# Optimization experiments

Measured on AMD Instinct MI355X. Metric: run time of the kernel, lower is better.

## Reference

```python
import jax, jax.numpy as jnp
import numpy as np


def setup_inputs() -> dict:
    key = jax.random.key(0)
    ks = jax.random.split(key, 6)
    B, N, Cd, Qd, E, G = 256, 196, 2048, 1024, 1024, 8
    s = lambda d: 1.0 / np.sqrt(d)
    return {
        "context": jax.random.normal(ks[0], (B, N, Cd), dtype=jnp.float32),
        "query": jax.random.normal(ks[1], (B, Qd), dtype=jnp.float32),
        "Wq": jax.random.normal(ks[2], (E, Qd), dtype=jnp.float32) * s(Qd),
        "bq": jnp.zeros((E,), dtype=jnp.float32),
        "Wc": jax.random.normal(ks[3], (E, Cd), dtype=jnp.float32) * s(Cd),
        "bc": jnp.zeros((E,), dtype=jnp.float32),
        "Wo": jax.random.normal(ks[4], (G, E), dtype=jnp.float32) * s(E),
        "bo": jnp.zeros((G,), dtype=jnp.float32),
    }


def reference(context, query, Wq, bq, Wc, bc, Wo, bo):
    # query: [B, Qd] -> [B, 1, E]; context: [B, N, Cd] -> [B, N, E]
    qp = (query @ Wq.T + bq)[:, None, :]
    cp = jnp.einsum('bnc,ec->bne', context, Wc) + bc
    # dropout in eval mode (identity)
    combined = jnp.tanh(qp + cp)                      # [B, N, E]
    attn = jnp.einsum('bne,ge->bng', combined, Wo) + bo  # [B, N, G]
    weights = jax.nn.softmax(attn, axis=1)            # softmax over regions
    glimpses = jnp.einsum('bng,bnc->bgc', weights, context)  # [B, G, Cd]
    return glimpses.reshape(context.shape[0], -1)     # [B, G*Cd]
```

## Files before the change

### kernel.cpp

```cpp
#include <hip/hip_runtime.h>
#include <stdint.h>

typedef unsigned int u32;
typedef __bf16 bf16_t;
typedef bf16_t bf16x8 __attribute__((ext_vector_type(8)));
typedef bf16_t bf16x4 __attribute__((ext_vector_type(4)));
typedef float  f32x4  __attribute__((ext_vector_type(4)));

#define NB   256
#define NN   196
#define CD   2048
#define QD   1024
#define NE   1024
#define NG   8

#define WS_QP    0
#define WS_ATTN  (NB*NE*4)
#define WS_WCB   (WS_ATTN + NB*NG*NN*4)

__device__ __forceinline__ bf16_t f2bf(float f){
  u32 u = __float_as_uint(f);
  u += 0x7fffu + ((u >> 16) & 1u);
  unsigned short h = (unsigned short)(u >> 16);
  return __builtin_bit_cast(bf16_t, h);
}

__device__ __forceinline__ float fast_tanh(float x){
  float e = __expf(2.0f * x);
  return 1.0f - 2.0f / (e + 1.0f);
}

__device__ __forceinline__ void load_lds16(const void* g, void* l){
  __builtin_amdgcn_global_load_lds(
      (const __attribute__((address_space(1))) void*)g,
      (__attribute__((address_space(3))) void*)l, 16, 0, 0);
}

__global__ __launch_bounds__(256)
void k_conv(const float* __restrict__ src, bf16_t* __restrict__ dst){
  size_t i = ((size_t)blockIdx.x * 256 + threadIdx.x) * 4;
  float4 v = *(const float4*)(src + i);
  bf16x4 o = { f2bf(v.x), f2bf(v.y), f2bf(v.z), f2bf(v.w) };
  *(bf16x4*)(dst + i) = o;
}

__global__ __launch_bounds__(256)
void k_qp(const float* __restrict__ query, const float* __restrict__ Wq,
          const float* __restrict__ bq, float* __restrict__ qp){
  __shared__ float qs[32][36];
  __shared__ float wsm[32][36];
  const u32 t  = threadIdx.x;
  const u32 e0 = blockIdx.x * 32, b0 = blockIdx.y * 32;
  const u32 r  = t >> 3, ci = (t & 7) * 4;
  const u32 tm = (t >> 4) * 2, tn = (t & 15) * 2;
  float c00 = 0.f, c01 = 0.f, c10 = 0.f, c11 = 0.f;
  for (u32 k0 = 0; k0 < QD; k0 += 32){
    float4 qv = *(const float4*)(query + (size_t)(b0 + r) * QD + k0 + ci);
    float4 wv = *(const float4*)(Wq    + (size_t)(e0 + r) * QD + k0 + ci);
    __syncthreads();
    *(float4*)&qs[r][ci]  = qv;
    *(float4*)&wsm[r][ci] = wv;
    __syncthreads();
    #pragma unroll
    for (int kq = 0; kq < 8; kq++){
      float4 a0 = *(const float4*)&qs[tm][kq*4];
      float4 a1 = *(const float4*)&qs[tm+1][kq*4];
      float4 b0v = *(const float4*)&wsm[tn][kq*4];
      float4 b1v = *(const float4*)&wsm[tn+1][kq*4];
      c00 += a0.x*b0v.x + a0.y*b0v.y + a0.z*b0v.z + a0.w*b0v.w;
      c01 += a0.x*b1v.x + a0.y*b1v.y + a0.z*b1v.z + a0.w*b1v.w;
      c10 += a1.x*b0v.x + a1.y*b0v.y + a1.z*b0v.z + a1.w*b0v.w;
      c11 += a1.x*b1v.x + a1.y*b1v.y + a1.z*b1v.z + a1.w*b1v.w;
    }
  }
  float bq0 = bq[e0+tn], bq1 = bq[e0+tn+1];
  qp[(size_t)(b0+tm  )*NE + e0+tn  ] = c00 + bq0;
  qp[(size_t)(b0+tm  )*NE + e0+tn+1] = c01 + bq1;
  qp[(size_t)(b0+tm+1)*NE + e0+tn  ] = c10 + bq0;
  qp[(size_t)(b0+tm+1)*NE + e0+tn+1] = c11 + bq1;
}

#define BM 128
#define BN 128
#define BK 32
#define KSTEPS (CD/BK)

__global__ __launch_bounds__(256, 3)
void k_mainA(const float* __restrict__ ctx, const bf16_t* __restrict__ wcb,
             const float* __restrict__ qp, const float* __restrict__ bcv,
             const float* __restrict__ Wo, float* __restrict__ attn)
{
  __shared__ char smem[49152] __attribute__((aligned(128)));

  const u32 tid  = threadIdx.x;
  const u32 lane = tid & 63;
  const u32 wave = tid >> 6;
  const u32 wm   = wave >> 1;
  const u32 wn   = wave & 1;

  u32 d  = blockIdx.x;
  u32 x  = d & 7;
  u32 s  = d >> 3;
  u32 ec = s & 7;
  u32 j  = s >> 3;
  u32 ms = j * 8 + x;
  const u32 m0 = ms * BM;
  const u32 e0 = ec * BN;

  const u32 arow = tid >> 3;
  const u32 aq   = (tid & 7) ^ (arow & 7);
  const float* aS = ctx + (size_t)(m0 + arow) * CD + aq * 4;
  char* aD = smem + tid * 16;

  const u32 brow0 = tid >> 2;
  const u32 brow1 = (tid + 256) >> 2;
  const u32 bkq0  = (tid & 3) ^ ((tid >> 3) & 3);
  const u32 bkq1  = (tid & 3) ^ (((tid + 256) >> 3) & 3);
  const bf16_t* bS0 = wcb + (size_t)(e0 + brow0) * CD + bkq0 * 8;
  const bf16_t* bS1 = wcb + (size_t)(e0 + brow1) * CD + bkq1 * 8;
  char* bD0 = smem + 32768 + tid * 16;
  char* bD1 = bD0 + 4096;

  f32x4 acc[4][4];
  #pragma unroll
  for (int i = 0; i < 4; i++)
    #pragma unroll
    for (int jn = 0; jn < 4; jn++) acc[i][jn] = (f32x4){0.f,0.f,0.f,0.f};

  auto stage = [&](u32 buf, u32 ks){
    const u32 ko = ks * BK;
    #pragma unroll
    for (int p = 0; p < 4; p++)
      load_lds16(aS + (size_t)(p * 32) * CD + ko, aD + buf * 16384u + p * 4096u);
    load_lds16(bS0 + ko, bD0 + buf * 8192u);
    load_lds16(bS1 + ko, bD1 + buf * 8192u);
  };

  const u32 q   = lane >> 4;
  const u32 r15 = lane & 15;
  const u32 as0 = ((2*q)     ^ (r15 & 7)) * 16;
  const u32 as1 = ((2*q + 1) ^ (r15 & 7)) * 16;
  const u32 bsw = (q ^ ((r15 >> 1) & 3)) * 16;

  auto compute = [&](u32 buf){
    const char* A = smem + buf * 16384u;
    const char* B = smem + 32768u + buf * 8192u;
    bf16x8 af[4], bfr[4];
    #pragma unroll
    for (int mt = 0; mt < 4; mt++){
      u32 row = wm*64 + mt*16 + r15;
      const char* rb = A + row * 128u;
      f32x4 lo = *(const f32x4*)(rb + as0);
      f32x4 hi = *(const f32x4*)(rb + as1);
      bf16x8 v = { (bf16_t)lo[0], (bf16_t)lo[1], (bf16_t)lo[2], (bf16_t)lo[3],
                   (bf16_t)hi[0], (bf16_t)hi[1], (bf16_t)hi[2], (bf16_t)hi[3] };
      af[mt] = v;
    }
    #pragma unroll
    for (int nt = 0; nt < 4; nt++){
      u32 row = wn*64 + nt*16 + r15;
      bfr[nt] = *(const bf16x8*)(B + row*64 + bsw);
    }
    #pragma unroll
    for (int mt = 0; mt < 4; mt++)
      #pragma unroll
      for (int nt = 0; nt < 4; nt++)
        acc[mt][nt] = __builtin_amdgcn_mfma_f32_16x16x32_bf16(af[mt], bfr[nt], acc[mt][nt], 0, 0, 0);
  };

  stage(0, 0);
  __syncthreads();
  for (u32 ks = 0; ks < KSTEPS; ks++){
    if (ks + 1 < KSTEPS) stage((ks + 1) & 1, ks + 1);
    compute(ks & 1);
    __syncthreads();
  }

  float*  qp0  = (float*)(smem + 35840);
  float*  qp1  = (float*)(smem + 36352);
  float*  bcs  = (float*)(smem + 36864);
  bf16_t* comb = (bf16_t*)smem;

  const u32 b0  = m0 / 196u;
  const u32 bnd = (b0 + 1) * 196u - m0;

  if (tid < 128){
    qp0[tid] = qp[(size_t)b0 * NE + e0 + tid];
    bcs[tid] = bcv[e0 + tid];
  } else {
    u32 b1 = b0 + 1; if (b1 >= NB) b1 = NB - 1;
    qp1[tid - 128] = qp[(size_t)b1 * NE + e0 + (tid - 128)];
  }

  bf16x8 wf[4];
  {
    u32 g = lane & 15;
    #pragma unroll
    for (int kk = 0; kk < 4; kk++){
      #pragma unroll
      for (int rr = 0; rr < 8; rr++){
        u32 ei = e0 + kk*32 + q*8 + rr;
        float v = (g < NG) ? Wo[(size_t)g * NE + ei] : 0.0f;
        wf[kk][rr] = f2bf(v);
      }
    }
  }
  __syncthreads();

  #pragma unroll
  for (int nt = 0; nt < 4; nt++){
    u32 el = wn*64 + nt*16 + r15;
    float qa = qp0[el];
    float qb = qp1[el];
    float bcx = bcs[el];
    #pragma unroll
    for (int mt = 0; mt < 4; mt++){
      u32 rl = wm*64 + mt*16 + q*4;
      #pragma unroll
      for (int r = 0; r < 4; r++){
        u32 row = rl + r;
        float qv = (row >= bnd) ? qb : qa;
        float t = fast_tanh(acc[mt][nt][r] + qv + bcx);
        comb[row*136 + el] = f2bf(t);
      }
    }
  }
  __syncthreads();

  #pragma unroll
  for (int i = 0; i < 2; i++){
    u32 nrow = (wave*2 + i)*16 + r15;
    f32x4 at = (f32x4){0.f,0.f,0.f,0.f};
    #pragma unroll
    for (int kk = 0; kk < 4; kk++){
      bf16x8 cf = *(const bf16x8*)&comb[nrow*136 + kk*32 + q*8];
      at = __builtin_amdgcn_mfma_f32_16x16x32_bf16(wf[kk], cf, at, 0, 0, 0);
    }
    if (q < 2){
      u32 mrow = m0 + nrow;
      u32 bb = mrow / 196u;
      u32 nn = mrow - bb * 196u;
      #pragma unroll
      for (int r = 0; r < 4; r++){
        u32 g = q*4 + r;
        atomicAdd(&attn[((size_t)bb * NG + g) * NN + nn], at[r]);
      }
    }
  }
}

__global__ __launch_bounds__(256)
void k_softmax(float* __restrict__ attn){
  u32 flat = blockIdx.x * 4 + (threadIdx.x >> 6);
  u32 lane = threadIdx.x & 63;
  float* row = attn + (size_t)flat * NN;
  float v0 = row[lane];
  float v1 = row[lane + 64];
  float v2 = row[lane + 128];
  float v3 = (lane < 4) ? row[lane + 192] : -1e30f;
  float m = fmaxf(fmaxf(v0, v1), fmaxf(v2, v3));
  #pragma unroll
  for (int o = 1; o < 64; o <<= 1) m = fmaxf(m, __shfl_xor(m, o));
  float e0 = __expf(v0 - m), e1 = __expf(v1 - m), e2 = __expf(v2 - m);
  float e3 = (lane < 4) ? __expf(v3 - m) : 0.f;
  float sum = e0 + e1 + e2 + e3;
  #pragma unroll
  for (int o = 1; o < 64; o <<= 1) sum += __shfl_xor(sum, o);
  float inv = 1.0f / sum;
  row[lane]       = e0 * inv;
  row[lane + 64]  = e1 * inv;
  row[lane + 128] = e2 * inv;
  if (lane < 4) row[lane + 192] = e3 * inv;
}

__global__ __launch_bounds__(256)
void k_glimpse(const float* __restrict__ ctx, const float* __restrict__ w,
               float* __restrict__ out){
  const u32 b  = blockIdx.y;
  const u32 c0 = blockIdx.x * 512 + threadIdx.x * 2;
  __shared__ float ws_[NG * NN];
  for (u32 i = threadIdx.x; i < NG * NN; i += 256)
    ws_[i] = w[(size_t)b * NG * NN + i];
  __syncthreads();
  const float* cp = ctx + (size_t)b * NN * CD + c0;
  float2 acc[NG];
  #pragma unroll
  for (int g = 0; g < NG; g++) acc[g] = make_float2(0.f, 0.f);
  for (u32 n = 0; n < NN; n++){
    float2 v = *(const float2*)(cp + (size_t)n * CD);
    #pragma unroll
    for (int g = 0; g < NG; g++){
      float wv = ws_[g * NN + n];
      acc[g].x = fmaf(wv, v.x, acc[g].x);
      acc[g].y = fmaf(wv, v.y, acc[g].y);
    }
  }
  #pragma unroll
  for (int g = 0; g < NG; g++)
    *(float2*)(out + (size_t)b * (NG * CD) + (size_t)g * CD + c0) = acc[g];
}

extern "C" void kernel_launch(void* const* d_in, const int* in_sizes, int n_in,
                              void* d_out, int out_size, void* d_ws, size_t ws_size,
                              hipStream_t stream)
{
  const float* ctx   = (const float*)d_in[0];
  const float* query = (const float*)d_in[1];
  const float* Wq    = (const float*)d_in[2];
  const float* bq    = (const float*)d_in[3];
  const float* Wc    = (const float*)d_in[4];
  const float* bc    = (const float*)d_in[5];
  const float* Wo    = (const float*)d_in[6];

  char* ws = (char*)d_ws;
  float*  qp   = (float*)(ws + WS_QP);
  float*  attn = (float*)(ws + WS_ATTN);
  bf16_t* wcb  = (bf16_t*)(ws + WS_WCB);
  float*  out  = (float*)d_out;

  (void)hipMemsetAsync(attn, 0, (size_t)NB * NG * NN * 4, stream);
  k_conv<<<2048, 256, 0, stream>>>(Wc, wcb);
  k_qp<<<dim3(32, 8), 256, 0, stream>>>(query, Wq, bq, qp);
  k_mainA<<<3136, 256, 0, stream>>>(ctx, wcb, qp, bc, Wo, attn);
  k_softmax<<<512, 256, 0, stream>>>(attn);
  k_glimpse<<<dim3(4, 256), 256, 0, stream>>>(ctx, attn, out);
}
```

Measured before the change: 480.5 us.

## Pre-convert context to bf16 and widen main GEMM tile to 128x256

Adds a separate kernel that converts the whole fp32 context tensor to bf16 in workspace. The main fused GEMM+tanh+Wo kernel then loads bf16 A tiles directly, with no in-loop fp32-to-bf16 conversion. Its N tile grows from 128 to 256, which halves the number of times context is re-read across E chunks and doubles the accumulators per wave. The cost is an extra full pass over context (read fp32, write bf16) and more registers and LDS per block, which lowers occupancy to 2 blocks per CU.

```diff
diff --git a/kernel.cpp b/kernel.cpp
--- a/kernel.cpp
+++ b/kernel.cpp
@@ -17,6 +17,7 @@
 #define WS_QP    0
 #define WS_ATTN  (NB*NE*4)
 #define WS_WCB   (WS_ATTN + NB*NG*NN*4)
+#define WS_CTXB  (WS_WCB + (size_t)NE*CD*2)
 
 __device__ __forceinline__ bf16_t f2bf(float f){
   u32 u = __float_as_uint(f);
@@ -42,6 +43,16 @@
   float4 v = *(const float4*)(src + i);
   bf16x4 o = { f2bf(v.x), f2bf(v.y), f2bf(v.z), f2bf(v.w) };
   *(bf16x4*)(dst + i) = o;
+}
+
+__global__ __launch_bounds__(256)
+void k_convctx(const float* __restrict__ src, bf16_t* __restrict__ dst){
+  size_t i = ((size_t)blockIdx.x * 256 + threadIdx.x) * 8;
+  float4 a = *(const float4*)(src + i);
+  float4 b = *(const float4*)(src + i + 4);
+  bf16x8 o = { f2bf(a.x), f2bf(a.y), f2bf(a.z), f2bf(a.w),
+               f2bf(b.x), f2bf(b.y), f2bf(b.z), f2bf(b.w) };
+  *(bf16x8*)(dst + i) = o;
 }
 
 __global__ __launch_bounds__(256)
@@ -81,16 +92,16 @@
 }
 
 #define BM 128
-#define BN 128
+#define BN 256
 #define BK 32
 #define KSTEPS (CD/BK)
 
-__global__ __launch_bounds__(256, 3)
-void k_mainA(const float* __restrict__ ctx, const bf16_t* __restrict__ wcb,
-             const float* __restrict__ qp, const float* __restrict__ bcv,
-             const float* __restrict__ Wo, float* __restrict__ attn)
+__global__ __launch_bounds__(256, 2)
+void k_main256(const bf16_t* __restrict__ ctxb, const bf16_t* __restrict__ wcb,
+               const float* __restrict__ qp, const float* __restrict__ bcv,
+               const float* __restrict__ Wo, float* __restrict__ attn)
 {
-  __shared__ char smem[49152] __attribute__((aligned(128)));
+  __shared__ char smem[70656] __attribute__((aligned(128)));
 
   const u32 tid  = threadIdx.x;
   const u32 lane = tid & 63;
@@ -101,70 +112,62 @@
   u32 d  = blockIdx.x;
   u32 x  = d & 7;
   u32 s  = d >> 3;
-  u32 ec = s & 7;
-  u32 j  = s >> 3;
+  u32 ec = s & 3;
+  u32 j  = s >> 2;
   u32 ms = j * 8 + x;
   const u32 m0 = ms * BM;
   const u32 e0 = ec * BN;
 
-  const u32 arow = tid >> 3;
-  const u32 aq   = (tid & 7) ^ (arow & 7);
-  const float* aS = ctx + (size_t)(m0 + arow) * CD + aq * 4;
+  const u32 srow = tid >> 2;
+  const u32 kqs  = (tid & 3) ^ ((tid >> 3) & 3);
+
+  const bf16_t* aS0 = ctxb + (size_t)(m0 + srow) * CD + kqs * 8;
+  const bf16_t* aS1 = aS0 + (size_t)64 * CD;
+  const bf16_t* bS0 = wcb  + (size_t)(e0 + srow) * CD + kqs * 8;
+  const bf16_t* bS1 = bS0 + (size_t)64  * CD;
+  const bf16_t* bS2 = bS0 + (size_t)128 * CD;
+  const bf16_t* bS3 = bS0 + (size_t)192 * CD;
   char* aD = smem + tid * 16;
-
-  const u32 brow0 = tid >> 2;
-  const u32 brow1 = (tid + 256) >> 2;
-  const u32 bkq0  = (tid & 3) ^ ((tid >> 3) & 3);
-  const u32 bkq1  = (tid & 3) ^ (((tid + 256) >> 3) & 3);
-  const bf16_t* bS0 = wcb + (size_t)(e0 + brow0) * CD + bkq0 * 8;
-  const bf16_t* bS1 = wcb + (size_t)(e0 + brow1) * CD + bkq1 * 8;
-  char* bD0 = smem + 32768 + tid * 16;
-  char* bD1 = bD0 + 4096;
-
-  f32x4 acc[4][4];
+  char* bD = smem + 16384 + tid * 16;
+
+  f32x4 acc[4][8];
   #pragma unroll
   for (int i = 0; i < 4; i++)
     #pragma unroll
-    for (int jn = 0; jn < 4; jn++) acc[i][jn] = (f32x4){0.f,0.f,0.f,0.f};
+    for (int jn = 0; jn < 8; jn++) acc[i][jn] = (f32x4){0.f,0.f,0.f,0.f};
 
   auto stage = [&](u32 buf, u32 ks){
     const u32 ko = ks * BK;
-    #pragma unroll
-    for (int p = 0; p < 4; p++)
-      load_lds16(aS + (size_t)(p * 32) * CD + ko, aD + buf * 16384u + p * 4096u);
-    load_lds16(bS0 + ko, bD0 + buf * 8192u);
-    load_lds16(bS1 + ko, bD1 + buf * 8192u);
+    load_lds16(aS0 + ko, aD + buf * 8192u);
+    load_lds16(aS1 + ko, aD + buf * 8192u + 4096u);
+    load_lds16(bS0 + ko, bD + buf * 16384u);
+    load_lds16(bS1 + ko, bD + buf * 16384u + 4096u);
+    load_lds16(bS2 + ko, bD + buf * 16384u + 8192u);
+    load_lds16(bS3 + ko, bD + buf * 16384u + 12288u);
   };
 
   const u32 q   = lane >> 4;
   const u32 r15 = lane & 15;
-  const u32 as0 = ((2*q)     ^ (r15 & 7)) * 16;
-  const u32 as1 = ((2*q + 1) ^ (r15 & 7)) * 16;
-  const u32 bsw = (q ^ ((r15 >> 1) & 3)) * 16;
+  const u32 sw  = (q ^ ((r15 >> 1) & 3)) * 16;
 
   auto compute = [&](u32 buf){
-    const char* A = smem + buf * 16384u;
-    const char* B = smem + 32768u + buf * 8192u;
-    bf16x8 af[4], bfr[4];
+    const char* A = smem + buf * 8192u;
+    const char* B = smem + 16384u + buf * 16384u;
+    bf16x8 af[4], bfr[8];
     #pragma unroll
     for (int mt = 0; mt < 4; mt++){
       u32 row = wm*64 + mt*16 + r15;
-      const char* rb = A + row * 128u;
-      f32x4 lo = *(const f32x4*)(rb + as0);
-      f32x4 hi = *(const f32x4*)(rb + as1);
-      bf16x8 v = { (bf16_t)lo[0], (bf16_t)lo[1], (bf16_t)lo[2], (bf16_t)lo[3],
-                   (bf16_t)hi[0], (bf16_t)hi[1], (bf16_t)hi[2], (bf16_t)hi[3] };
-      af[mt] = v;
-    }
-    #pragma unroll
-    for (int nt = 0; nt < 4; nt++){
-      u32 row = wn*64 + nt*16 + r15;
-      bfr[nt] = *(const bf16x8*)(B + row*64 + bsw);
+      af[mt] = *(const bf16x8*)(A + row*64 + sw);
+    }
+    #pragma unroll
+    for (int nt = 0; nt < 8; nt++){
+      u32 row = wn*128 + nt*16 + r15;
+      bfr[nt] = *(const bf16x8*)(B + row*64 + sw);
     }
     #pragma unroll
     for (int mt = 0; mt < 4; mt++)
       #pragma unroll
-      for (int nt = 0; nt < 4; nt++)
+      for (int nt = 0; nt < 8; nt++)
         acc[mt][nt] = __builtin_amdgcn_mfma_f32_16x16x32_bf16(af[mt], bfr[nt], acc[mt][nt], 0, 0, 0);
   };
 
@@ -176,27 +179,24 @@
     __syncthreads();
   }
 
-  float*  qp0  = (float*)(smem + 35840);
-  float*  qp1  = (float*)(smem + 36352);
-  float*  bcs  = (float*)(smem + 36864);
+  float*  qp0  = (float*)(smem + 67584);
+  float*  qp1  = (float*)(smem + 68608);
+  float*  bcs  = (float*)(smem + 69632);
   bf16_t* comb = (bf16_t*)smem;
 
   const u32 b0  = m0 / 196u;
   const u32 bnd = (b0 + 1) * 196u - m0;
-
-  if (tid < 128){
-    qp0[tid] = qp[(size_t)b0 * NE + e0 + tid];
-    bcs[tid] = bcv[e0 + tid];
-  } else {
-    u32 b1 = b0 + 1; if (b1 >= NB) b1 = NB - 1;
-    qp1[tid - 128] = qp[(size_t)b1 * NE + e0 + (tid - 128)];
-  }
-
-  bf16x8 wf[4];
+  u32 b1 = b0 + 1; if (b1 >= NB) b1 = NB - 1;
+
+  qp0[tid] = qp[(size_t)b0 * NE + e0 + tid];
+  qp1[tid] = qp[(size_t)b1 * NE + e0 + tid];
+  bcs[tid] = bcv[e0 + tid];
+
+  bf16x8 wf[8];
   {
-    u32 g = lane & 15;
-    #pragma unroll
-    for (int kk = 0; kk < 4; kk++){
+    u32 g = r15;
+    #pragma unroll
+    for (int kk = 0; kk < 8; kk++){
       #pragma unroll
       for (int rr = 0; rr < 8; rr++){
         u32 ei = e0 + kk*32 + q*8 + rr;
@@ -208,8 +208,8 @@
   __syncthreads();
 
   #pragma unroll
-  for (int nt = 0; nt < 4; nt++){
-    u32 el = wn*64 + nt*16 + r15;
+  for (int nt = 0; nt < 8; nt++){
+    u32 el = wn*128 + nt*16 + r15;
     float qa = qp0[el];
     float qb = qp1[el];
     float bcx = bcs[el];
@@ -221,7 +221,7 @@
         u32 row = rl + r;
         float qv = (row >= bnd) ? qb : qa;
         float t = fast_tanh(acc[mt][nt][r] + qv + bcx);
-        comb[row*136 + el] = f2bf(t);
+        comb[row*264 + el] = f2bf(t);
       }
     }
   }
@@ -232,8 +232,8 @@
     u32 nrow = (wave*2 + i)*16 + r15;
     f32x4 at = (f32x4){0.f,0.f,0.f,0.f};
     #pragma unroll
-    for (int kk = 0; kk < 4; kk++){
-      bf16x8 cf = *(const bf16x8*)&comb[nrow*136 + kk*32 + q*8];
+    for (int kk = 0; kk < 8; kk++){
+      bf16x8 cf = *(const bf16x8*)&comb[nrow*264 + kk*32 + q*8];
       at = __builtin_amdgcn_mfma_f32_16x16x32_bf16(wf[kk], cf, at, 0, 0, 0);
     }
     if (q < 2){
@@ -316,12 +316,14 @@
   float*  qp   = (float*)(ws + WS_QP);
   float*  attn = (float*)(ws + WS_ATTN);
   bf16_t* wcb  = (bf16_t*)(ws + WS_WCB);
+  bf16_t* ctxb = (bf16_t*)(ws + WS_CTXB);
   float*  out  = (float*)d_out;
 
   (void)hipMemsetAsync(attn, 0, (size_t)NB * NG * NN * 4, stream);
   k_conv<<<2048, 256, 0, stream>>>(Wc, wcb);
   k_qp<<<dim3(32, 8), 256, 0, stream>>>(query, Wq, bq, qp);
-  k_mainA<<<3136, 256, 0, stream>>>(ctx, wcb, qp, bc, Wo, attn);
+  k_convctx<<<50176, 256, 0, stream>>>(ctx, ctxb);
+  k_main256<<<1568, 256, 0, stream>>>(ctxb, wcb, qp, bc, Wo, attn);
   k_softmax<<<512, 256, 0, stream>>>(attn);
   k_glimpse<<<dim3(4, 256), 256, 0, stream>>>(ctx, attn, out);
 }
```

Measured after the change: 497.1 us. +3.5%, slower.

## Load context tile directly into registers instead of staging through LDS

Applied to the files above, without the earlier changes.

The fp32 context (A operand) tile is now prefetched from global memory straight into registers one k-step ahead, using a two-buffer register ping-pong, instead of being staged through LDS with async loads. Only the bf16 Wc tile still goes through LDS, which cuts shared memory use from 48KB to 36KB. This removes the LDS write and read traffic for A. In exchange it adds vector registers for the prefetch buffers and leaves global load latency exposed to register pressure. Each wave also reloads A rows that the other wave sharing those rows fetches too, which duplicates global or L2 traffic.

```diff
diff --git a/kernel.cpp b/kernel.cpp
--- a/kernel.cpp
+++ b/kernel.cpp
@@ -86,11 +86,11 @@
 #define KSTEPS (CD/BK)
 
 __global__ __launch_bounds__(256, 3)
-void k_mainA(const float* __restrict__ ctx, const bf16_t* __restrict__ wcb,
+void k_mainB(const float* __restrict__ ctx, const bf16_t* __restrict__ wcb,
              const float* __restrict__ qp, const float* __restrict__ bcv,
              const float* __restrict__ Wo, float* __restrict__ attn)
 {
-  __shared__ char smem[49152] __attribute__((aligned(128)));
+  __shared__ char smem[36864] __attribute__((aligned(128)));
 
   const u32 tid  = threadIdx.x;
   const u32 lane = tid & 63;
@@ -107,10 +107,10 @@
   const u32 m0 = ms * BM;
   const u32 e0 = ec * BN;
 
-  const u32 arow = tid >> 3;
-  const u32 aq   = (tid & 7) ^ (arow & 7);
-  const float* aS = ctx + (size_t)(m0 + arow) * CD + aq * 4;
-  char* aD = smem + tid * 16;
+  const u32 q   = lane >> 4;
+  const u32 r15 = lane & 15;
+
+  const float* aBase = ctx + (size_t)(m0 + wm*64 + r15) * CD + q * 8;
 
   const u32 brow0 = tid >> 2;
   const u32 brow1 = (tid + 256) >> 2;
@@ -118,7 +118,7 @@
   const u32 bkq1  = (tid & 3) ^ (((tid + 256) >> 3) & 3);
   const bf16_t* bS0 = wcb + (size_t)(e0 + brow0) * CD + bkq0 * 8;
   const bf16_t* bS1 = wcb + (size_t)(e0 + brow1) * CD + bkq1 * 8;
-  char* bD0 = smem + 32768 + tid * 16;
+  char* bD0 = smem + tid * 16;
   char* bD1 = bD0 + 4096;
 
   f32x4 acc[4][4];
@@ -127,58 +127,68 @@
     #pragma unroll
     for (int jn = 0; jn < 4; jn++) acc[i][jn] = (f32x4){0.f,0.f,0.f,0.f};
 
-  auto stage = [&](u32 buf, u32 ks){
+  auto stageB = [&](u32 buf, u32 ks){
     const u32 ko = ks * BK;
-    #pragma unroll
-    for (int p = 0; p < 4; p++)
-      load_lds16(aS + (size_t)(p * 32) * CD + ko, aD + buf * 16384u + p * 4096u);
     load_lds16(bS0 + ko, bD0 + buf * 8192u);
     load_lds16(bS1 + ko, bD1 + buf * 8192u);
   };
 
-  const u32 q   = lane >> 4;
-  const u32 r15 = lane & 15;
-  const u32 as0 = ((2*q)     ^ (r15 & 7)) * 16;
-  const u32 as1 = ((2*q + 1) ^ (r15 & 7)) * 16;
   const u32 bsw = (q ^ ((r15 >> 1) & 3)) * 16;
 
-  auto compute = [&](u32 buf){
-    const char* A = smem + buf * 16384u;
-    const char* B = smem + 32768u + buf * 8192u;
-    bf16x8 af[4], bfr[4];
-    #pragma unroll
-    for (int mt = 0; mt < 4; mt++){
-      u32 row = wm*64 + mt*16 + r15;
-      const char* rb = A + row * 128u;
-      f32x4 lo = *(const f32x4*)(rb + as0);
-      f32x4 hi = *(const f32x4*)(rb + as1);
-      bf16x8 v = { (bf16_t)lo[0], (bf16_t)lo[1], (bf16_t)lo[2], (bf16_t)lo[3],
-                   (bf16_t)hi[0], (bf16_t)hi[1], (bf16_t)hi[2], (bf16_t)hi[3] };
-      af[mt] = v;
-    }
-    #pragma unroll
-    for (int nt = 0; nt < 4; nt++){
-      u32 row = wn*64 + nt*16 + r15;
-      bfr[nt] = *(const bf16x8*)(B + row*64 + bsw);
-    }
-    #pragma unroll
-    for (int mt = 0; mt < 4; mt++)
-      #pragma unroll
-      for (int nt = 0; nt < 4; nt++)
-        acc[mt][nt] = __builtin_amdgcn_mfma_f32_16x16x32_bf16(af[mt], bfr[nt], acc[mt][nt], 0, 0, 0);
-  };
-
-  stage(0, 0);
+  f32x4 avA[4][2], avB[4][2];
+
+#define PREF_A(DST, KS) do{                                                     \
+    const float* p_ = aBase + (size_t)(KS) * BK;                                \
+    _Pragma("unroll")                                                           \
+    for (int mt = 0; mt < 4; mt++){                                             \
+      DST[mt][0] = *(const f32x4*)(p_ + (size_t)mt * 16 * CD);                  \
+      DST[mt][1] = *(const f32x4*)(p_ + (size_t)mt * 16 * CD + 4);              \
+    }                                                                           \
+  }while(0)
+
+#define COMPUTE(BUF, SRC) do{                                                   \
+    const char* B_ = smem + (BUF) * 8192u;                                      \
+    bf16x8 af[4], bfr[4];                                                       \
+    _Pragma("unroll")                                                           \
+    for (int mt = 0; mt < 4; mt++){                                             \
+      af[mt] = (bf16x8){ (bf16_t)SRC[mt][0][0], (bf16_t)SRC[mt][0][1],          \
+                         (bf16_t)SRC[mt][0][2], (bf16_t)SRC[mt][0][3],          \
+                         (bf16_t)SRC[mt][1][0], (bf16_t)SRC[mt][1][1],          \
+                         (bf16_t)SRC[mt][1][2], (bf16_t)SRC[mt][1][3] };        \
+    }                                                                           \
+    _Pragma("unroll")                                                           \
+    for (int nt = 0; nt < 4; nt++){                                             \
+      u32 row_ = wn*64 + nt*16 + r15;                                           \
+      bfr[nt] = *(const bf16x8*)(B_ + row_*64 + bsw);                           \
+    }                                                                           \
+    _Pragma("unroll")                                                           \
+    for (int mt = 0; mt < 4; mt++)                                              \
+      _Pragma("unroll")                                                         \
+      for (int nt = 0; nt < 4; nt++)                                            \
+        acc[mt][nt] = __builtin_amdgcn_mfma_f32_16x16x32_bf16(                  \
+            af[mt], bfr[nt], acc[mt][nt], 0, 0, 0);                             \
+  }while(0)
+
+  PREF_A(avA, 0);
+  stageB(0, 0);
   __syncthreads();
-  for (u32 ks = 0; ks < KSTEPS; ks++){
-    if (ks + 1 < KSTEPS) stage((ks + 1) & 1, ks + 1);
-    compute(ks & 1);
+
+  for (u32 ks = 0; ks < KSTEPS; ks += 2){
+    stageB((ks + 1) & 1, ks + 1);
+    PREF_A(avB, ks + 1);
+    COMPUTE(ks & 1, avA);
     __syncthreads();
-  }
-
-  float*  qp0  = (float*)(smem + 35840);
-  float*  qp1  = (float*)(smem + 36352);
-  float*  bcs  = (float*)(smem + 36864);
+    if (ks + 2 < KSTEPS){
+      stageB((ks + 2) & 1, ks + 2);
+      PREF_A(avA, ks + 2);
+    }
+    COMPUTE((ks + 1) & 1, avB);
+    __syncthreads();
+  }
+
+  float*  qp0  = (float*)(smem + 34816);
+  float*  qp1  = (float*)(smem + 35328);
+  float*  bcs  = (float*)(smem + 35840);
   bf16_t* comb = (bf16_t*)smem;
 
   const u32 b0  = m0 / 196u;
@@ -321,7 +331,7 @@
   (void)hipMemsetAsync(attn, 0, (size_t)NB * NG * NN * 4, stream);
   k_conv<<<2048, 256, 0, stream>>>(Wc, wcb);
   k_qp<<<dim3(32, 8), 256, 0, stream>>>(query, Wq, bq, qp);
-  k_mainA<<<3136, 256, 0, stream>>>(ctx, wcb, qp, bc, Wo, attn);
+  k_mainB<<<3136, 256, 0, stream>>>(ctx, wcb, qp, bc, Wo, attn);
   k_softmax<<<512, 256, 0, stream>>>(attn);
   k_glimpse<<<dim3(4, 256), 256, 0, stream>>>(ctx, attn, out);
 }
```

Measured after the change: 945.1 us. 96.7% more time.
